# Optimization experiments

Measured on AMD Instinct MI355X. Metric: run time of the kernel, lower is better.

## Reference

```python
import jax, jax.numpy as jnp
import numpy as np

BN_EPS = 1e-5
K = 3  # number of nearest neighbors for interpolation


def _square_distance(src, dst):
    # src: [B,N,3], dst: [B,S,3] -> [B,N,S]
    d = -2.0 * jnp.einsum('bnc,bsc->bns', src, dst)
    d = d + jnp.sum(src * src, axis=-1)[:, :, None]
    d = d + jnp.sum(dst * dst, axis=-1)[:, None, :]
    return d


def _conv_bn_relu(x, w, b, gamma, beta):
    # x: [B,C,N], w: [O,C], b: [O]
    y = jnp.einsum('bcn,oc->bon', x, w) + b[None, :, None]
    mean = jnp.mean(y, axis=(0, 2), keepdims=True)
    var = jnp.var(y, axis=(0, 2), keepdims=True)
    y = (y - mean) * jax.lax.rsqrt(var + BN_EPS)
    y = y * gamma[None, :, None] + beta[None, :, None]
    return jax.nn.relu(y)


def setup_inputs() -> dict:
    key = jax.random.key(0)
    ks = jax.random.split(key, 12)
    B, N, S, D1, D2 = 8, 8192, 2048, 256, 256
    Cin = D1 + D2
    xyz1 = jax.random.normal(ks[0], (B, N, 3), dtype=jnp.float32)
    xyz2 = jax.random.normal(ks[1], (B, S, 3), dtype=jnp.float32)
    points1 = jax.random.normal(ks[2], (B, D1, N), dtype=jnp.float32)
    points2 = jax.random.normal(ks[3], (B, D2, S), dtype=jnp.float32)
    w1 = jax.random.normal(ks[4], (256, Cin), dtype=jnp.float32) * (1.0 / np.sqrt(Cin))
    b1 = jnp.zeros((256,), dtype=jnp.float32)
    g1 = jnp.ones((256,), dtype=jnp.float32)
    be1 = jnp.zeros((256,), dtype=jnp.float32)
    w2 = jax.random.normal(ks[5], (256, 256), dtype=jnp.float32) * (1.0 / np.sqrt(256))
    b2 = jnp.zeros((256,), dtype=jnp.float32)
    g2 = jnp.ones((256,), dtype=jnp.float32)
    be2 = jnp.zeros((256,), dtype=jnp.float32)
    return {"xyz1": xyz1, "xyz2": xyz2, "points1": points1, "points2": points2,
            "w1": w1, "b1": b1, "g1": g1, "be1": be1,
            "w2": w2, "b2": b2, "g2": g2, "be2": be2}


def reference(xyz1, xyz2, points1, points2, w1, b1, g1, be1, w2, b2, g2, be2):
    B, N, _ = xyz1.shape
    dists = _square_distance(xyz1, xyz2)              # [B,N,S]
    neg_d, idx = jax.lax.top_k(-dists, K)             # 3 smallest distances
    d3 = -neg_d                                       # [B,N,3]
    dist_recip = 1.0 / (d3 + 1e-8)
    weight = dist_recip / jnp.sum(dist_recip, axis=2, keepdims=True)  # [B,N,3]
    p2 = jnp.swapaxes(points2, 1, 2)                  # [B,S,D2]
    gathered = jax.vmap(lambda pts, ix: pts[ix])(p2, idx)  # [B,N,3,D2]
    interp = jnp.sum(gathered * weight[..., None], axis=2)  # [B,N,D2]
    new_points = jnp.concatenate([jnp.swapaxes(points1, 1, 2), interp], axis=-1)  # [B,N,D1+D2]
    x = jnp.swapaxes(new_points, 1, 2)                # [B,Cin,N]
    x = _conv_bn_relu(x, w1, b1, g1, be1)
    x = _conv_bn_relu(x, w2, b2, g2, be2)
    return x
```

## Files before the change

### kernel.cpp

```cpp
#include <hip/hip_runtime.h>
#include <hip/hip_bf16.h>
#include <float.h>

#define BB 8
#define NNq 8192
#define SSk 2048
#define CIN 512
#define OC 256
#define NR (BB * NNq)
#define NBX 512
#define KNN_HALF 1024

typedef __attribute__((ext_vector_type(8))) short bf16x8;
typedef __attribute__((ext_vector_type(8))) unsigned short ushort8;
typedef __attribute__((ext_vector_type(4))) float f32x4;
typedef __attribute__((ext_vector_type(2))) float f32x2;

__device__ __forceinline__ unsigned short f2bf(float f) {
  union { __hip_bfloat16 h; unsigned short u; } v;
  v.h = __float2bfloat16(f);
  return v.u;
}
__device__ __forceinline__ float bf2f(unsigned short u) {
  union { unsigned int i; float f; } x; x.i = ((unsigned int)u) << 16; return x.f;
}

__device__ __forceinline__ f32x2 pkdist(f32x2 xp, f32x2 yp, f32x2 zp, f32x2 pp2,
                                        f32x2 cxy, f32x2 czw) {
  f32x2 t, m;
  asm("v_pk_mul_f32 %0, %2, %6 op_sel:[0,0] op_sel_hi:[1,0]\n\t"
      "v_pk_mul_f32 %1, %3, %6 op_sel:[0,1] op_sel_hi:[1,1]\n\t"
      "v_pk_add_f32 %0, %0, %1\n\t"
      "v_pk_mul_f32 %1, %4, %7 op_sel:[0,0] op_sel_hi:[1,0]\n\t"
      "v_pk_add_f32 %0, %0, %1\n\t"
      "v_pk_add_f32 %0, %0, %5\n\t"
      "v_pk_add_f32 %0, %0, %7 op_sel:[0,1] op_sel_hi:[1,1]"
      : "=&v"(t), "=&v"(m)
      : "v"(xp), "v"(yp), "v"(zp), "v"(pp2), "v"(cxy), "v"(czw));
  return t;
}

__device__ __forceinline__ void insert3(float d, int ix, float& e0, float& e1, float& e2,
                                        int& i0, int& i1, int& i2) {
  int t;
  asm("v_cmp_lt_f32 vcc, %[d], %[e2]\n\t"
      "v_cndmask_b32 %[t], %[i2], %[ix], vcc\n\t"
      "v_cmp_lt_f32 vcc, %[d], %[e1]\n\t"
      "v_cndmask_b32 %[i2], %[t], %[i1], vcc\n\t"
      "v_cndmask_b32 %[t], %[i1], %[ix], vcc\n\t"
      "v_cmp_lt_f32 vcc, %[d], %[e0]\n\t"
      "v_cndmask_b32 %[i1], %[t], %[i0], vcc\n\t"
      "v_cndmask_b32 %[i0], %[i0], %[ix], vcc\n\t"
      "v_med3_f32 %[e2], %[d], %[e1], %[e2]\n\t"
      "v_med3_f32 %[e1], %[d], %[e0], %[e1]\n\t"
      "v_min_f32 %[e0], %[e0], %[d]"
      : [e0]"+v"(e0), [e1]"+v"(e1), [e2]"+v"(e2),
        [i0]"+v"(i0), [i1]"+v"(i1), [i2]"+v"(i2), [t]"=&v"(t)
      : [d]"v"(d), [ix]"v"(ix)
      : "vcc");
}

__global__ __launch_bounds__(512) void k_front(const float* __restrict__ xyz1,
                                               const float* __restrict__ xyz2,
                                               const float* __restrict__ p1,
                                               const float* __restrict__ p2,
                                               const float* __restrict__ w1,
                                               const float* __restrict__ w2,
                                               float* __restrict__ pe, int* __restrict__ pi,
                                               __hip_bfloat16* __restrict__ xb,
                                               float* __restrict__ p2t,
                                               __hip_bfloat16* __restrict__ wb1,
                                               __hip_bfloat16* __restrict__ wb2) {
  __shared__ char sm[24576];
  int id = blockIdx.x;
  int type, sub;
  if (id < 2048)       { type = (id & 1) ? 1 : 0; sub = id >> 1; }
  else if (id < 9216)  { type = 1; sub = 1024 + (id - 2048); }
  else if (id < 11264) { type = 2; sub = id - 9216; }
  else                 { type = 3; sub = id - 11264; }

  if (type == 0) {
    float4* lsh = (float4*)sm;
    float* meP = (float*)sm;
    int*   miP = (int*)sm + 3072;
    int qblk = sub & 63, b = (sub >> 6) & 7, half = sub >> 9;
    int t = threadIdx.x;
    int lane = t & 63, w = t >> 6;

#pragma unroll
    for (int j = 0; j < 2; ++j) {
      int p = t + j * 512;
      const float* s = xyz2 + ((long)b * SSk + half * KNN_HALF + p) * 3;
      float x = s[0], y = s[1], z = s[2];
      float qq = __fadd_rn(__fadd_rn(__fmul_rn(x, x), __fmul_rn(y, y)), __fmul_rn(z, z));
      lsh[p] = make_float4(-2.f * x, -2.f * y, -2.f * z, qq);
    }

    long baseA = (long)b * NNq + qblk * 128 + lane;
    long baseB = baseA + 64;
    float xa = xyz1[baseA * 3 + 0], ya = xyz1[baseA * 3 + 1], za = xyz1[baseA * 3 + 2];
    float xb_ = xyz1[baseB * 3 + 0], yb_ = xyz1[baseB * 3 + 1], zb_ = xyz1[baseB * 3 + 2];
    float ppa = __fadd_rn(__fadd_rn(__fmul_rn(xa, xa), __fmul_rn(ya, ya)), __fmul_rn(za, za));
    float ppb = __fadd_rn(__fadd_rn(__fmul_rn(xb_, xb_), __fmul_rn(yb_, yb_)), __fmul_rn(zb_, zb_));
    f32x2 xp = {xa, xb_}, yp = {ya, yb_}, zp = {za, zb_}, pp2 = {ppa, ppb};
    __syncthreads();

    float e0a = FLT_MAX, e1a = FLT_MAX, e2a = FLT_MAX;
    float e0b = FLT_MAX, e1b = FLT_MAX, e2b = FLT_MAX;
    int i0a = 0, i1a = 0, i2a = 0, i0b = 0, i1b = 0, i2b = 0;
    const f32x4* __restrict__ qp = (const f32x4*)(lsh + w * 128);
#pragma unroll 8
    for (int ii = 0; ii < 128; ++ii) {
      f32x4 c = qp[ii];
      f32x2 d2 = pkdist(xp, yp, zp, pp2, c.xy, c.zw);
      insert3(d2.x, ii, e0a, e1a, e2a, i0a, i1a, i2a);
      insert3(d2.y, ii, e0b, e1b, e2b, i0b, i1b, i2b);
    }
    __syncthreads();
    int s0 = half * KNN_HALF + w * 128;
    meP[(w * 3 + 0) * 128 + lane] = e0a; meP[(w * 3 + 1) * 128 + lane] = e1a; meP[(w * 3 + 2) * 128 + lane] = e2a;
    meP[(w * 3 + 0) * 128 + 64 + lane] = e0b; meP[(w * 3 + 1) * 128 + 64 + lane] = e1b; meP[(w * 3 + 2) * 128 + 64 + lane] = e2b;
    miP[(w * 3 + 0) * 128 + lane] = i0a + s0; miP[(w * 3 + 1) * 128 + lane] = i1a + s0; miP[(w * 3 + 2) * 128 + lane] = i2a + s0;
    miP[(w * 3 + 0) * 128 + 64 + lane] = i0b + s0; miP[(w * 3 + 1) * 128 + 64 + lane] = i1b + s0; miP[(w * 3 + 2) * 128 + 64 + lane] = i2b + s0;
    __syncthreads();

    if (t < 128) {
      float e0 = meP[0 * 128 + t], e1 = meP[1 * 128 + t], e2 = meP[2 * 128 + t];
      int   g0 = miP[0 * 128 + t], g1 = miP[1 * 128 + t], g2 = miP[2 * 128 + t];
      for (int ww = 1; ww < 8; ++ww) {
#pragma unroll
        for (int k = 0; k < 3; ++k) {
          float d = meP[(ww * 3 + k) * 128 + t]; int s = miP[(ww * 3 + k) * 128 + t];
          if (d < e2) {
            if (d < e1) {
              e2 = e1; g2 = g1;
              if (d < e0) { e1 = e0; g1 = g0; e0 = d; g0 = s; }
              else        { e1 = d; g1 = s; }
            } else { e2 = d; g2 = s; }
          }
        }
      }
      long base = (long)b * NNq + qblk * 128 + t;
      long o = ((long)half * NR + base) * 3;
      pe[o + 0] = e0; pe[o + 1] = e1; pe[o + 2] = e2;
      pi[o + 0] = g0; pi[o + 1] = g1; pi[o + 2] = g2;
    }
  } else if (type == 1) {
    int th = threadIdx.x & 255, hsub = threadIdx.x >> 8;
    float (*T)[33] = (float(*)[33])((float*)sm + hsub * (32 * 33));
    int b = sub >> 10, c0 = ((sub >> 7) & 7) * 32, n0 = (sub & 127) * 64 + hsub * 32;
    int tx = th & 31, ty = th >> 5;
#pragma unroll
    for (int r = 0; r < 32; r += 8)
      T[ty + r][tx] = p1[((long)(b * 256 + c0 + ty + r)) * NNq + n0 + tx];
    __syncthreads();
#pragma unroll
    for (int r = 0; r < 32; r += 8)
      xb[((long)(b * NNq + n0 + ty + r)) * CIN + c0 + tx] = __float2bfloat16(T[tx][ty + r]);
  } else if (type == 2) {
    int th = threadIdx.x & 255, hsub = threadIdx.x >> 8;
    float (*T)[33] = (float(*)[33])((float*)sm + hsub * (32 * 33));
    int b = sub >> 8, c0 = ((sub >> 5) & 7) * 32, s0 = (sub & 31) * 64 + hsub * 32;
    int tx = th & 31, ty = th >> 5;
#pragma unroll
    for (int r = 0; r < 32; r += 8)
      T[ty + r][tx] = p2[((long)(b * 256 + c0 + ty + r)) * SSk + s0 + tx];
    __syncthreads();
#pragma unroll
    for (int r = 0; r < 32; r += 8)
      p2t[((long)(b * SSk + s0 + ty + r)) * 256 + c0 + tx] = T[tx][ty + r];
  } else {
    int i = sub * 512 + threadIdx.x;
    if (i < 131072) wb1[i] = __float2bfloat16(w1[i]);
    else            wb2[i - 131072] = __float2bfloat16(w2[i - 131072]);
  }
}

__global__ void k_gather(const float* __restrict__ p2t, const float* __restrict__ pe,
                         const int* __restrict__ pi, __hip_bfloat16* __restrict__ xb) {
  int b = blockIdx.y;
  int wid = threadIdx.x >> 6, lane = threadIdx.x & 63;
  int n = blockIdx.x * 4 + wid;
  long t = (long)b * NNq + n;
  float e0 = pe[t * 3 + 0], e1 = pe[t * 3 + 1], e2 = pe[t * 3 + 2];
  int   g0 = pi[t * 3 + 0], g1 = pi[t * 3 + 1], g2 = pi[t * 3 + 2];
  long o1 = ((long)NR + t) * 3;
#pragma unroll
  for (int k = 0; k < 3; ++k) {
    float d = pe[o1 + k]; int s = pi[o1 + k];
    if (d < e2) {
      if (d < e1) {
        e2 = e1; g2 = g1;
        if (d < e0) { e1 = e0; g1 = g0; e0 = d; g0 = s; }
        else        { e1 = d; g1 = s; }
      } else { e2 = d; g2 = s; }
    }
  }
  float r0 = 1.f / (e0 + 1e-8f), r1 = 1.f / (e1 + 1e-8f), r2 = 1.f / (e2 + 1e-8f);
  float rs = r0 + r1 + r2;
  float w0 = r0 / rs, w1 = r1 / rs, w2 = r2 / rs;

  const float4* q0 = (const float4*)(p2t + ((long)(b * SSk + g0)) * 256);
  const float4* q1 = (const float4*)(p2t + ((long)(b * SSk + g1)) * 256);
  const float4* q2 = (const float4*)(p2t + ((long)(b * SSk + g2)) * 256);
  float4 a = q0[lane], c = q1[lane], d = q2[lane];
  float vx = w0 * a.x + w1 * c.x + w2 * d.x;
  float vy = w0 * a.y + w1 * c.y + w2 * d.y;
  float vz = w0 * a.z + w1 * c.z + w2 * d.z;
  float vw = w0 * a.w + w1 * c.w + w2 * d.w;
  ushort4 u;
  u.x = f2bf(vx); u.y = f2bf(vy); u.z = f2bf(vz); u.w = f2bf(vw);
  *(ushort4*)((unsigned short*)xb + t * CIN + 256 + lane * 4) = u;
}

template <int K>
__global__ __launch_bounds__(256) void k_gemm(const __hip_bfloat16* __restrict__ X,
                                              const __hip_bfloat16* __restrict__ W,
                                              unsigned short* __restrict__ Yb,
                                              float* __restrict__ part) {
  constexpr int BK = 32;
  __shared__ __hip_bfloat16 xT[128 * BK];
  __shared__ __hip_bfloat16 wT[128 * BK];
  __shared__ float sb[4][4][16], qb[4][4][16];
  const int id = blockIdx.x;
  const int super = id >> 4, slot = id & 15;
  const int bx = super * 8 + (slot & 7);
  const int r0 = bx * 128;
  const int c0 = (slot >> 3) * 128;
  const int tid = threadIdx.x;
  const int wid = tid >> 6, lane = tid & 63;
  const int wr = wid >> 1, wc = wid & 1;
  f32x4 acc[4][4] = {};

  for (int kt = 0; kt < K; kt += BK) {
#pragma unroll
    for (int jj = 0; jj < 2; ++jj) {
      int j = wid * 2 + jj;
      int row = j * 16 + (lane >> 2);
      const __hip_bfloat16* g = X + ((long)(r0 + row)) * K + kt + (lane & 3) * 8;
      __builtin_amdgcn_global_load_lds((const __attribute__((address_space(1))) void*)(const void*)g,
                                       (__attribute__((address_space(3))) void*)(void*)(xT + j * 512),
                                       16, 0, 0);
    }
#pragma unroll
    for (int jj = 0; jj < 2; ++jj) {
      int j = wid * 2 + jj;
      int row = j * 16 + (lane >> 2);
      const __hip_bfloat16* g = W + ((long)(c0 + row)) * K + kt + (lane & 3) * 8;
      __builtin_amdgcn_global_load_lds((const __attribute__((address_space(1))) void*)(const void*)g,
                                       (__attribute__((address_space(3))) void*)(void*)(wT + j * 512),
                                       16, 0, 0);
    }
    __syncthreads();

    bf16x8 af[4], bfr[4];
#pragma unroll
    for (int m = 0; m < 4; ++m) {
      int row = wr * 64 + m * 16 + (lane & 15);
      af[m] = *(const bf16x8*)(xT + row * BK + (lane >> 4) * 8);
    }
#pragma unroll
    for (int nn = 0; nn < 4; ++nn) {
      int row = wc * 64 + nn * 16 + (lane & 15);
      bfr[nn] = *(const bf16x8*)(wT + row * BK + (lane >> 4) * 8);
    }
#pragma unroll
    for (int m = 0; m < 4; ++m)
#pragma unroll
      for (int nn = 0; nn < 4; ++nn)
        acc[m][nn] = __builtin_amdgcn_mfma_f32_16x16x32_bf16(af[m], bfr[nn], acc[m][nn], 0, 0, 0);
    __syncthreads();
  }

#pragma unroll
  for (int m = 0; m < 4; ++m)
#pragma unroll
    for (int nn = 0; nn < 4; ++nn)
#pragma unroll
      for (int reg = 0; reg < 4; ++reg) {
        int r = r0 + wr * 64 + m * 16 + (lane >> 4) * 4 + reg;
        int c = c0 + wc * 64 + nn * 16 + (lane & 15);
        Yb[(long)r * OC + c] = f2bf(acc[m][nn][reg]);
      }

#pragma unroll
  for (int nn = 0; nn < 4; ++nn) {
    float s = 0.f, q = 0.f;
#pragma unroll
    for (int m = 0; m < 4; ++m)
#pragma unroll
      for (int reg = 0; reg < 4; ++reg) {
        float v = acc[m][nn][reg];
        s += v; q += v * v;
      }
    s += __shfl_xor(s, 16); s += __shfl_xor(s, 32);
    q += __shfl_xor(q, 16); q += __shfl_xor(q, 32);
    if (lane < 16) { sb[wid][nn][lane] = s; qb[wid][nn][lane] = q; }
  }
  __syncthreads();
  if (tid < 128) {
    int col = tid & 15, nn = (tid >> 4) & 3, wcc = (tid >> 6) & 1;
    float s = sb[wcc][nn][col] + sb[2 + wcc][nn][col];
    float q = qb[wcc][nn][col] + qb[2 + wcc][nn][col];
    int ch = c0 + wcc * 64 + nn * 16 + col;
    part[(long)ch * NBX + bx] = s;
    part[(long)(256 + ch) * NBX + bx] = q;
  }
}

__global__ void k_scalefix(const float* __restrict__ part, const float* __restrict__ g,
                           const float* __restrict__ be, float* __restrict__ st) {
  __shared__ float sred[8][33], qred[8][33];
  int ch_l = threadIdx.x >> 5, j = threadIdx.x & 31;
  int o = blockIdx.x * 8 + ch_l;
  const float4* ps = (const float4*)(part + (long)o * NBX + j * 16);
  const float4* pq = (const float4*)(part + (long)(256 + o) * NBX + j * 16);
  float s = 0.f, q = 0.f;
#pragma unroll
  for (int i = 0; i < 4; ++i) {
    float4 a = ps[i], bq = pq[i];
    s += (a.x + a.y) + (a.z + a.w);
    q += (bq.x + bq.y) + (bq.z + bq.w);
  }
  sred[ch_l][j] = s; qred[ch_l][j] = q;
  __syncthreads();
  if (threadIdx.x < 8) {
    int ch = threadIdx.x;
    float ss = 0.f, qq = 0.f;
#pragma unroll
    for (int i = 0; i < 32; ++i) { ss += sred[ch][i]; qq += qred[ch][i]; }
    int oo = blockIdx.x * 8 + ch;
    float mean = ss * (1.f / NR);
    float var = qq * (1.f / NR) - mean * mean;
    float sc = g[oo] * rsqrtf(var + 1e-5f);
    st[oo] = sc;
    st[OC + oo] = be[oo] - mean * sc;
  }
}

__global__ void k_bnrelu_bf16(const unsigned short* __restrict__ Y, const float* __restrict__ st,
                              unsigned short* __restrict__ Yb) {
  long i8 = (long)blockIdx.x * 256 + threadIdx.x;
  ushort8 v = ((const ushort8*)Y)[i8];
  int c8 = (int)(i8 & 31);
  float4 sca = ((const float4*)st)[c8 * 2];
  float4 scb = ((const float4*)st)[c8 * 2 + 1];
  float4 sha = ((const float4*)(st + OC))[c8 * 2];
  float4 shb = ((const float4*)(st + OC))[c8 * 2 + 1];
  ushort8 u;
  u[0] = f2bf(fmaxf(fmaf(bf2f(v[0]), sca.x, sha.x), 0.f));
  u[1] = f2bf(fmaxf(fmaf(bf2f(v[1]), sca.y, sha.y), 0.f));
  u[2] = f2bf(fmaxf(fmaf(bf2f(v[2]), sca.z, sha.z), 0.f));
  u[3] = f2bf(fmaxf(fmaf(bf2f(v[3]), sca.w, sha.w), 0.f));
  u[4] = f2bf(fmaxf(fmaf(bf2f(v[4]), scb.x, shb.x), 0.f));
  u[5] = f2bf(fmaxf(fmaf(bf2f(v[5]), scb.y, shb.y), 0.f));
  u[6] = f2bf(fmaxf(fmaf(bf2f(v[6]), scb.z, shb.z), 0.f));
  u[7] = f2bf(fmaxf(fmaf(bf2f(v[7]), scb.w, shb.w), 0.f));
  ((ushort8*)Yb)[i8] = u;
}

__global__ void k_final(const unsigned short* __restrict__ Y, const float* __restrict__ st,
                        float* __restrict__ out) {
  __shared__ float tile[256][33];
  int b = blockIdx.z, o0 = blockIdx.y * 32, n0 = blockIdx.x * 256;
  int t = threadIdx.x;
  int cp = t & 15, tn = t >> 4;
  int c = cp * 2;
  float sc0 = st[o0 + c], sc1 = st[o0 + c + 1];
  float sh0 = st[OC + o0 + c], sh1 = st[OC + o0 + c + 1];
#pragma unroll
  for (int r = 0; r < 16; ++r) {
    int nl = r * 16 + tn;
    ushort2 v = *(const ushort2*)(Y + ((long)(b * NNq + n0 + nl)) * OC + o0 + c);
    tile[nl][c]     = fmaxf(fmaf(bf2f(v.x), sc0, sh0), 0.f);
    tile[nl][c + 1] = fmaxf(fmaf(bf2f(v.y), sc1, sh1), 0.f);
  }
  __syncthreads();
  int w = t >> 6, lane = t & 63;
#pragma unroll
  for (int rr = 0; rr < 8; ++rr) {
    int cl = w * 8 + rr;
    float4 v = make_float4(tile[lane * 4 + 0][cl], tile[lane * 4 + 1][cl],
                           tile[lane * 4 + 2][cl], tile[lane * 4 + 3][cl]);
    *(float4*)(out + ((long)(b * 256 + o0 + cl)) * NNq + n0 + lane * 4) = v;
  }
}

extern "C" void kernel_launch(void* const* d_in, const int* in_sizes, int n_in,
                              void* d_out, int out_size, void* d_ws, size_t ws_size,
                              hipStream_t stream) {
  const float* xyz1 = (const float*)d_in[0];
  const float* xyz2 = (const float*)d_in[1];
  const float* p1   = (const float*)d_in[2];
  const float* p2   = (const float*)d_in[3];
  const float* w1   = (const float*)d_in[4];
  const float* g1   = (const float*)d_in[6];
  const float* be1  = (const float*)d_in[7];
  const float* w2   = (const float*)d_in[8];
  const float* g2   = (const float*)d_in[10];
  const float* be2  = (const float*)d_in[11];
  float* out = (float*)d_out;

  char* ws = (char*)d_ws;
  const size_t OFF_XB   = 0;
  const size_t OFF_Y1   = 67108864;
  const size_t OFF_P2T  = OFF_Y1;
  const size_t OFF_PE   = OFF_Y1 + 16777216;
  const size_t OFF_PI   = OFF_PE + 1572864;
  const size_t OFF_MISC = 134217728;
  const size_t OFF_WB1  = OFF_MISC + 1835008;
  const size_t OFF_WB2  = OFF_MISC + 2097152;
  const size_t OFF_ST1  = OFF_MISC + 2228224;
  const size_t OFF_ST2  = OFF_MISC + 2230272;
  const size_t OFF_PART = OFF_MISC + 262144;

  __hip_bfloat16* xb   = (__hip_bfloat16*)(ws + OFF_XB);
  unsigned short* y1   = (unsigned short*)(ws + OFF_Y1);
  unsigned short* y2   = (unsigned short*)(ws + OFF_Y1);
  float* p2t           = (float*)(ws + OFF_P2T);
  float* pe            = (float*)(ws + OFF_PE);
  int*   pi            = (int*)(ws + OFF_PI);
  __hip_bfloat16* wb1  = (__hip_bfloat16*)(ws + OFF_WB1);
  __hip_bfloat16* wb2  = (__hip_bfloat16*)(ws + OFF_WB2);
  unsigned short* y1b  = (unsigned short*)(ws + OFF_XB);
  float* st1           = (float*)(ws + OFF_ST1);
  float* st2           = (float*)(ws + OFF_ST2);
  float* part          = (float*)(ws + OFF_PART);

  k_front<<<11648, 512, 0, stream>>>(xyz1, xyz2, p1, p2, w1, w2, pe, pi, xb, p2t, wb1, wb2);
  k_gather<<<dim3(NNq / 4, BB), 256, 0, stream>>>(p2t, pe, pi, xb);

  k_gemm<512><<<2 * NBX, 256, 0, stream>>>(xb, wb1, y1, part);
  k_scalefix<<<32, 256, 0, stream>>>(part, g1, be1, st1);
  k_bnrelu_bf16<<<(int)((long)NR * 256 / 8 / 256), 256, 0, stream>>>(y1, st1, y1b);

  k_gemm<256><<<2 * NBX, 256, 0, stream>>>((const __hip_bfloat16*)y1b, wb2, y2, part);
  k_scalefix<<<32, 256, 0, stream>>>(part, g2, be2, st2);
  k_final<<<dim3(NNq / 256, 256 / 32, BB), 256, 0, stream>>>(y2, st2, out);

  (void)in_sizes; (void)n_in; (void)out_size; (void)ws_size;
}
```

Baseline: 228.8 us.

## Process full KNN reference set per block and precompute interpolation weights

Each KNN block now scans all 2048 reference points, 256 per wave, instead of half of them. This removes the second-half partial results and the merge step from the gather kernel. The final top-3 indices and normalized inverse-distance weights are computed in the front kernel and written compactly, so the gather kernel only loads them. Block interleaving changes so KNN blocks are spread one per eight among transpose blocks. The trade-off is half as many KNN blocks, each with twice the work, which may lengthen the critical path of the KNN phase.

```diff
diff --git a/kernel.cpp b/kernel.cpp
--- a/kernel.cpp
+++ b/kernel.cpp
@@ -9,7 +9,6 @@
 #define OC 256
 #define NR (BB * NNq)
 #define NBX 512
-#define KNN_HALF 1024
 
 typedef __attribute__((ext_vector_type(8))) short bf16x8;
 typedef __attribute__((ext_vector_type(8))) unsigned short ushort8;
@@ -66,31 +65,35 @@
                                                const float* __restrict__ p2,
                                                const float* __restrict__ w1,
                                                const float* __restrict__ w2,
-                                               float* __restrict__ pe, int* __restrict__ pi,
+                                               int* __restrict__ idx3, float* __restrict__ w3,
                                                __hip_bfloat16* __restrict__ xb,
                                                float* __restrict__ p2t,
                                                __hip_bfloat16* __restrict__ wb1,
                                                __hip_bfloat16* __restrict__ wb2) {
-  __shared__ char sm[24576];
+  __shared__ char sm[32768];
   int id = blockIdx.x;
   int type, sub;
-  if (id < 2048)       { type = (id & 1) ? 1 : 0; sub = id >> 1; }
-  else if (id < 9216)  { type = 1; sub = 1024 + (id - 2048); }
-  else if (id < 11264) { type = 2; sub = id - 9216; }
-  else                 { type = 3; sub = id - 11264; }
+  if (id < 4096 && (id & 7) == 0) { type = 0; sub = id >> 3; }
+  else {
+    int s = (id < 4096) ? (id - (id >> 3) - 1) : (id - 512);
+    if (s < 8192)       { type = 1; sub = s; }
+    else if (s < 10240) { type = 2; sub = s - 8192; }
+    else if (s < 10624) { type = 3; sub = s - 10240; }
+    else return;
+  }
 
   if (type == 0) {
     float4* lsh = (float4*)sm;
     float* meP = (float*)sm;
     int*   miP = (int*)sm + 3072;
-    int qblk = sub & 63, b = (sub >> 6) & 7, half = sub >> 9;
+    int qblk = sub & 63, b = sub >> 6;
     int t = threadIdx.x;
     int lane = t & 63, w = t >> 6;
 
 #pragma unroll
-    for (int j = 0; j < 2; ++j) {
+    for (int j = 0; j < 4; ++j) {
       int p = t + j * 512;
-      const float* s = xyz2 + ((long)b * SSk + half * KNN_HALF + p) * 3;
+      const float* s = xyz2 + ((long)b * SSk + p) * 3;
       float x = s[0], y = s[1], z = s[2];
       float qq = __fadd_rn(__fadd_rn(__fmul_rn(x, x), __fmul_rn(y, y)), __fmul_rn(z, z));
       lsh[p] = make_float4(-2.f * x, -2.f * y, -2.f * z, qq);
@@ -108,16 +111,16 @@
     float e0a = FLT_MAX, e1a = FLT_MAX, e2a = FLT_MAX;
     float e0b = FLT_MAX, e1b = FLT_MAX, e2b = FLT_MAX;
     int i0a = 0, i1a = 0, i2a = 0, i0b = 0, i1b = 0, i2b = 0;
-    const f32x4* __restrict__ qp = (const f32x4*)(lsh + w * 128);
+    const f32x4* __restrict__ qp = (const f32x4*)(lsh + w * 256);
 #pragma unroll 8
-    for (int ii = 0; ii < 128; ++ii) {
+    for (int ii = 0; ii < 256; ++ii) {
       f32x4 c = qp[ii];
       f32x2 d2 = pkdist(xp, yp, zp, pp2, c.xy, c.zw);
       insert3(d2.x, ii, e0a, e1a, e2a, i0a, i1a, i2a);
       insert3(d2.y, ii, e0b, e1b, e2b, i0b, i1b, i2b);
     }
     __syncthreads();
-    int s0 = half * KNN_HALF + w * 128;
+    int s0 = w * 256;
     meP[(w * 3 + 0) * 128 + lane] = e0a; meP[(w * 3 + 1) * 128 + lane] = e1a; meP[(w * 3 + 2) * 128 + lane] = e2a;
     meP[(w * 3 + 0) * 128 + 64 + lane] = e0b; meP[(w * 3 + 1) * 128 + 64 + lane] = e1b; meP[(w * 3 + 2) * 128 + 64 + lane] = e2b;
     miP[(w * 3 + 0) * 128 + lane] = i0a + s0; miP[(w * 3 + 1) * 128 + lane] = i1a + s0; miP[(w * 3 + 2) * 128 + lane] = i2a + s0;
@@ -141,9 +144,10 @@
         }
       }
       long base = (long)b * NNq + qblk * 128 + t;
-      long o = ((long)half * NR + base) * 3;
-      pe[o + 0] = e0; pe[o + 1] = e1; pe[o + 2] = e2;
-      pi[o + 0] = g0; pi[o + 1] = g1; pi[o + 2] = g2;
+      float r0 = 1.f / (e0 + 1e-8f), r1 = 1.f / (e1 + 1e-8f), r2 = 1.f / (e2 + 1e-8f);
+      float rs = r0 + r1 + r2;
+      idx3[base * 3 + 0] = g0; idx3[base * 3 + 1] = g1; idx3[base * 3 + 2] = g2;
+      w3[base * 3 + 0] = r0 / rs; w3[base * 3 + 1] = r1 / rs; w3[base * 3 + 2] = r2 / rs;
     }
   } else if (type == 1) {
     int th = threadIdx.x & 255, hsub = threadIdx.x >> 8;
@@ -176,30 +180,15 @@
   }
 }
 
-__global__ void k_gather(const float* __restrict__ p2t, const float* __restrict__ pe,
-                         const int* __restrict__ pi, __hip_bfloat16* __restrict__ xb) {
+__global__ void k_gather(const float* __restrict__ p2t, const int* __restrict__ idx3,
+                         const float* __restrict__ w3, __hip_bfloat16* __restrict__ xb) {
   int b = blockIdx.y;
   int wid = threadIdx.x >> 6, lane = threadIdx.x & 63;
   int n = blockIdx.x * 4 + wid;
   long t = (long)b * NNq + n;
-  float e0 = pe[t * 3 + 0], e1 = pe[t * 3 + 1], e2 = pe[t * 3 + 2];
-  int   g0 = pi[t * 3 + 0], g1 = pi[t * 3 + 1], g2 = pi[t * 3 + 2];
-  long o1 = ((long)NR + t) * 3;
-#pragma unroll
-  for (int k = 0; k < 3; ++k) {
-    float d = pe[o1 + k]; int s = pi[o1 + k];
-    if (d < e2) {
-      if (d < e1) {
-        e2 = e1; g2 = g1;
-        if (d < e0) { e1 = e0; g1 = g0; e0 = d; g0 = s; }
-        else        { e1 = d; g1 = s; }
-      } else { e2 = d; g2 = s; }
-    }
-  }
-  float r0 = 1.f / (e0 + 1e-8f), r1 = 1.f / (e1 + 1e-8f), r2 = 1.f / (e2 + 1e-8f);
-  float rs = r0 + r1 + r2;
-  float w0 = r0 / rs, w1 = r1 / rs, w2 = r2 / rs;
-
+  long o = t * 3;
+  int g0 = idx3[o], g1 = idx3[o + 1], g2 = idx3[o + 2];
+  float w0 = w3[o], w1 = w3[o + 1], w2 = w3[o + 2];
   const float4* q0 = (const float4*)(p2t + ((long)(b * SSk + g0)) * 256);
   const float4* q1 = (const float4*)(p2t + ((long)(b * SSk + g1)) * 256);
   const float4* q2 = (const float4*)(p2t + ((long)(b * SSk + g2)) * 256);
@@ -405,21 +394,21 @@
   const size_t OFF_XB   = 0;
   const size_t OFF_Y1   = 67108864;
   const size_t OFF_P2T  = OFF_Y1;
-  const size_t OFF_PE   = OFF_Y1 + 16777216;
-  const size_t OFF_PI   = OFF_PE + 1572864;
   const size_t OFF_MISC = 134217728;
+  const size_t OFF_IDX  = OFF_MISC + 262144;
+  const size_t OFF_W3   = OFF_MISC + 1048576;
   const size_t OFF_WB1  = OFF_MISC + 1835008;
   const size_t OFF_WB2  = OFF_MISC + 2097152;
   const size_t OFF_ST1  = OFF_MISC + 2228224;
   const size_t OFF_ST2  = OFF_MISC + 2230272;
-  const size_t OFF_PART = OFF_MISC + 262144;
+  const size_t OFF_PART = OFF_IDX;
 
   __hip_bfloat16* xb   = (__hip_bfloat16*)(ws + OFF_XB);
   unsigned short* y1   = (unsigned short*)(ws + OFF_Y1);
   unsigned short* y2   = (unsigned short*)(ws + OFF_Y1);
   float* p2t           = (float*)(ws + OFF_P2T);
-  float* pe            = (float*)(ws + OFF_PE);
-  int*   pi            = (int*)(ws + OFF_PI);
+  int*   idx3          = (int*)(ws + OFF_IDX);
+  float* w3            = (float*)(ws + OFF_W3);
   __hip_bfloat16* wb1  = (__hip_bfloat16*)(ws + OFF_WB1);
   __hip_bfloat16* wb2  = (__hip_bfloat16*)(ws + OFF_WB2);
   unsigned short* y1b  = (unsigned short*)(ws + OFF_XB);
@@ -427,8 +416,8 @@
   float* st2           = (float*)(ws + OFF_ST2);
   float* part          = (float*)(ws + OFF_PART);
 
-  k_front<<<11648, 512, 0, stream>>>(xyz1, xyz2, p1, p2, w1, w2, pe, pi, xb, p2t, wb1, wb2);
-  k_gather<<<dim3(NNq / 4, BB), 256, 0, stream>>>(p2t, pe, pi, xb);
+  k_front<<<11264, 512, 0, stream>>>(xyz1, xyz2, p1, p2, w1, w2, idx3, w3, xb, p2t, wb1, wb2);
+  k_gather<<<dim3(NNq / 4, BB), 256, 0, stream>>>(p2t, idx3, w3, xb);
 
   k_gemm<512><<<2 * NBX, 256, 0, stream>>>(xb, wb1, y1, part);
   k_scalefix<<<32, 256, 0, stream>>>(part, g1, be1, st1);
```

Result: slower. 521.6 us (+128.0%).
